# Optimization experiments

Measured on AMD Instinct MI355X. Metric: run time of the kernel, lower is better.

The kernel has to match this reference:

```python
import jax, jax.numpy as jnp
import numpy as np

B, T, S = 64, 48, 48
E, H, L, V = 512, 1024, 2, 32000


def setup_inputs() -> dict:
    key = jax.random.key(0)
    ks = jax.random.split(key, 16)
    s = 0.02
    return {
        "tgt_input": jax.random.randint(ks[0], (B, T), 0, V),
        "h0": jax.random.normal(ks[1], (L, B, H), jnp.float32),
        "c0": jax.random.normal(ks[2], (L, B, H), jnp.float32),
        "encoder_output": jax.random.normal(ks[3], (B, S, H), jnp.float32),
        "src_key_padding_mask": jnp.zeros((B, S), bool),
        "embedding": jax.random.normal(ks[4], (V, E), jnp.float32) * s,
        "W_l": jax.random.normal(ks[5], (H, H), jnp.float32) * s,
        "b_l": jnp.zeros((H,), jnp.float32),
        "W_ih0": jax.random.normal(ks[6], (4 * H, E + H), jnp.float32) * s,
        "W_hh0": jax.random.normal(ks[7], (4 * H, H), jnp.float32) * s,
        "b_ih0": jnp.zeros((4 * H,), jnp.float32),
        "b_hh0": jnp.zeros((4 * H,), jnp.float32),
        "W_ih1": jax.random.normal(ks[8], (4 * H, H), jnp.float32) * s,
        "W_hh1": jax.random.normal(ks[9], (4 * H, H), jnp.float32) * s,
        "b_ih1": jnp.zeros((4 * H,), jnp.float32),
        "b_hh1": jnp.zeros((4 * H,), jnp.float32),
    }


def _lstm_cell(x, h, c, W_ih, W_hh, b_ih, b_hh):
    # PyTorch gate order: i, f, g, o
    gates = x @ W_ih.T + b_ih + h @ W_hh.T + b_hh  # [B, 4H]
    i, f, g, o = jnp.split(gates, 4, axis=-1)
    c_new = jax.nn.sigmoid(f) * c + jax.nn.sigmoid(i) * jnp.tanh(g)
    h_new = jax.nn.sigmoid(o) * jnp.tanh(c_new)
    return h_new, c_new


def reference(tgt_input, h0, c0, encoder_output, src_key_padding_mask,
              embedding, W_l, b_l,
              W_ih0, W_hh0, b_ih0, b_hh0,
              W_ih1, W_hh1, b_ih1, b_hh1):
    emb = embedding[tgt_input]              # [B, T, E]
    emb_t = jnp.transpose(emb, (1, 0, 2))   # [T, B, E]
    layers = ((W_ih0, W_hh0, b_ih0, b_hh0), (W_ih1, W_hh1, b_ih1, b_hh1))

    def step(carry, x_t):
        h, c = carry                        # [L, B, H] each
        # Luong attention with query = last-layer hidden state
        q = h[-1] @ W_l.T + b_l             # [B, H]
        scores = jnp.einsum('bh,bsh->bs', q, encoder_output)
        scores = jnp.where(src_key_padding_mask, -jnp.inf, scores)
        attn = jax.nn.softmax(scores, axis=-1)
        ctx = jnp.einsum('bs,bsh->bh', attn, encoder_output)  # [B, H]
        x = jnp.concatenate([x_t, ctx], axis=-1)              # [B, E+H]
        new_h, new_c = [], []
        for l, (W_ih, W_hh, b_ih, b_hh) in enumerate(layers):
            hn, cn = _lstm_cell(x, h[l], c[l], W_ih, W_hh, b_ih, b_hh)
            new_h.append(hn)
            new_c.append(cn)
            x = hn
        return (jnp.stack(new_h), jnp.stack(new_c)), x  # x = top-layer output

    (hn, cn), outs = jax.lax.scan(step, (h0, c0), emb_t)
    outputs = jnp.transpose(outs, (1, 0, 2))  # [B, T, H]
    return outputs, hn, cn
```

## Files before the change

kernel.cpp:

```cpp
#include <hip/hip_runtime.h>
#include <stdint.h>


using short8 = __attribute__((ext_vector_type(8))) short;
using f32x4  = __attribute__((ext_vector_type(4))) float;
typedef unsigned short u16;
typedef unsigned long long u64;

#define B_  64
#define T_  48
#define S_  48
#define H_  1024
#define E_  512

__device__ __forceinline__ float bf2f(u16 u) {
    union { unsigned int i; float f; } v; v.i = ((unsigned int)u) << 16; return v.f;
}
__device__ __forceinline__ u16 f2bf(float f) {
    union { float f; unsigned int i; } v; v.f = f;
    unsigned int r = v.i + 0x7fff + ((v.i >> 16) & 1);
    return (u16)(r >> 16);
}
__device__ __forceinline__ float sigm(float x) { return 1.f / (1.f + __expf(-x)); }


__global__ void cast_copy(u16* __restrict__ dst, int dld, int doff,
                          const float* __restrict__ src, int sld, int soff,
                          int rows, int colshift) {
    int cols = 1 << colshift;
    int total = rows << colshift;
    for (int i = blockIdx.x * blockDim.x + threadIdx.x; i < total;
         i += gridDim.x * blockDim.x) {
        int r = i >> colshift, c = i & (cols - 1);
        dst[(size_t)r * dld + doff + c] = f2bf(src[(size_t)r * sld + soff + c]);
    }
}

__global__ void transpose_cast(u16* __restrict__ dst, const float* __restrict__ src) {
    int idx = blockIdx.x * blockDim.x + threadIdx.x;
    int r = idx >> 10, c = idx & 1023;
    dst[idx] = f2bf(src[(size_t)c * 1024 + r]);
}

__global__ void embed_gather(u16* __restrict__ embA, const float* __restrict__ emb,
                             const int* __restrict__ tgt) {
    int row = blockIdx.x;
    int t = row >> 6, b = row & 63;
    int id = tgt[b * T_ + t];
    const float* s = emb + (size_t)id * E_;
    u16* d = embA + (size_t)row * E_;
    for (int e = threadIdx.x; e < E_; e += blockDim.x) d[e] = f2bf(s[e]);
}

__global__ void sbias_kernel(float* __restrict__ sbias, const float* __restrict__ enc,
                             const float* __restrict__ b_l) {
    int r = blockIdx.x, lane = threadIdx.x;
    const float* e = enc + (size_t)r * H_;
    float acc = 0.f;
    for (int k = lane; k < H_; k += 64) acc += b_l[k] * e[k];
    for (int o = 32; o; o >>= 1) acc += __shfl_xor(acc, o);
    if (lane == 0) sbias[r] = acc;
}

__global__ void init_state(u16* __restrict__ xa0_0, u16* __restrict__ xa1_0,
                           const float* __restrict__ h0) {
    int i = blockIdx.x * blockDim.x + threadIdx.x;
    int l = i >> 16, rem = i & 65535, b = rem >> 10, c = rem & 1023;
    u16 hb = f2bf(h0[i]);
    if (l == 0) xa0_0[b * 2048 + 1024 + c] = hb;
    else        xa1_0[b * 2048 + 1024 + c] = hb;
}

__global__ __launch_bounds__(256) void gemm64(
    const u16* __restrict__ A, const u16* __restrict__ W, u16* __restrict__ D,
    const float* __restrict__ bias1, const float* __restrict__ bias2,
    int N, int Kd)
{
    __shared__ float part[4][64][65];
    int tid = threadIdx.x, w = tid >> 6, lane = tid & 63;
    int hf = lane >> 4, q = lane & 15;
    int n0 = blockIdx.x * 64, m0 = blockIdx.y * 64;
    int ks = Kd >> 2;
    int kb = w * ks + hf * 8;
    const u16* ap = A + (size_t)(m0 + q) * Kd + kb;
    const u16* wp = W + (size_t)(n0 + q) * Kd + kb;
    f32x4 acc[4][4] = {};
    for (int k0 = 0; k0 < ks; k0 += 32) {
        short8 bf[4], af[4];
#pragma unroll
        for (int n = 0; n < 4; ++n) bf[n] = *(const short8*)(wp + (size_t)n * 16 * Kd + k0);
#pragma unroll
        for (int m = 0; m < 4; ++m) af[m] = *(const short8*)(ap + (size_t)m * 16 * Kd + k0);
#pragma unroll
        for (int m = 0; m < 4; ++m)
#pragma unroll
            for (int n = 0; n < 4; ++n)
                acc[m][n] = __builtin_amdgcn_mfma_f32_16x16x32_bf16(af[m], bf[n], acc[m][n], 0, 0, 0);
    }
#pragma unroll
    for (int m = 0; m < 4; ++m)
#pragma unroll
        for (int n = 0; n < 4; ++n)
#pragma unroll
            for (int r = 0; r < 4; ++r)
                part[w][m * 16 + hf * 4 + r][n * 16 + q] = acc[m][n][r];
    __syncthreads();
#pragma unroll
    for (int k = 0; k < 16; ++k) {
        int o = tid + k * 256;
        int row = o >> 6, col = o & 63;
        float v = part[0][row][col] + part[1][row][col]
                + part[2][row][col] + part[3][row][col];
        if (bias1) v += bias1[n0 + col] + bias2[n0 + col];
        D[(size_t)(m0 + row) * N + n0 + col] = f2bf(v);
    }
}


struct PParams {
    const float *W_ih0, *W_hh0, *W_ih1, *W_hh1;
    const u16  *preG, *encW, *encB;
    const float *sbias, *b_ih1, *b_hh1, *c0in;
    const unsigned char* mask;
    u16 *XA0, *XA1;
    float *out, *hn0, *hn1, *cn0, *cn1;
    unsigned *cnt, *flags;
};

__device__ __forceinline__ void gridbar(unsigned* cnt, unsigned* flags, int ep) {
    __syncthreads();
    const int tid = threadIdx.x;
    const int g = (blockIdx.x & 7) * 8 + ((blockIdx.x >> 3) & 7);
    if (tid == 0)
        __hip_atomic_fetch_add(&cnt[g * 256 + ep], 1u,
                               __ATOMIC_RELAXED, __HIP_MEMORY_SCOPE_AGENT);
    if (blockIdx.x == 0) {
        if (tid < 64) {
            int spin = 0;
            for (;;) {
                unsigned v = __hip_atomic_load(&cnt[tid * 256 + ep],
                                               __ATOMIC_RELAXED,
                                               __HIP_MEMORY_SCOPE_AGENT);
                if (__ballot(v >= 4u) == ~0ull) break;
                __builtin_amdgcn_s_sleep(1);
                if (++spin > (1 << 20)) break;
            }
            __hip_atomic_store(&flags[tid * 256 + ep], 1u,
                               __ATOMIC_RELAXED, __HIP_MEMORY_SCOPE_AGENT);
        }
    } else if (tid == 0) {
        int spin = 0;
        while (!__hip_atomic_load(&flags[g * 256 + ep], __ATOMIC_RELAXED,
                                  __HIP_MEMORY_SCOPE_AGENT)) {
            __builtin_amdgcn_s_sleep(1);
            if (++spin > (1 << 20)) break;
        }
    }
    asm volatile("" ::: "memory");
    __syncthreads();
}

__global__ void __launch_bounds__(256, 1) decoder_persistent(PParams P) {
    __shared__ u16 wlds[2][4096][8];
    __shared__ union {
        struct { float h1f[1056]; float sc[48][4]; float pr[48]; } at;
        float gates[64][20];
    } sm;

    const int tid = threadIdx.x, blk = blockIdx.x;
    const int w = tid >> 6, lane = tid & 63, g4 = lane >> 4, q = lane & 15;
    const int b2 = tid >> 2, j2 = tid & 3;
    const int colg = blk * 4 + j2;

    {
        int r = tid & 15, cb = tid >> 4;
        int grow = (r >> 2) * 1024 + blk * 4 + (r & 3);
#pragma unroll
        for (int l = 0; l < 2; ++l) {
            const float* Sa = l ? P.W_ih1 : P.W_ih0;
            const float* Sb = l ? P.W_hh1 : P.W_hh0;
            int sld  = l ? 1024 : 1536;
            int soff = l ? 0 : 512;
            for (int it = 0; it < 16; ++it) {
                int c = cb + it * 16;
                int k = c * 8;
                const float* src = (k < 1024)
                    ? (Sa + (size_t)grow * sld + soff + k)
                    : (Sb + (size_t)grow * 1024 + (k - 1024));
                float4 x0 = *(const float4*)(src);
                float4 x1 = *(const float4*)(src + 4);
                short8 v;
                v[0] = f2bf(x0.x); v[1] = f2bf(x0.y); v[2] = f2bf(x0.z); v[3] = f2bf(x0.w);
                v[4] = f2bf(x1.x); v[5] = f2bf(x1.y); v[6] = f2bf(x1.z); v[7] = f2bf(x1.w);
                *(short8*)&wlds[l][c * 16 + r][0] = v;
            }
        }
    }
    float bsum[4];
#pragma unroll
    for (int g = 0; g < 4; ++g)
        bsum[g] = P.b_ih1[g * 1024 + colg] + P.b_hh1[g * 1024 + colg];
    float c0r = P.c0in[b2 * 1024 + colg];
    float c1r = P.c0in[65536 + b2 * 1024 + colg];

    const int ab = (blk & 7) * 8 + ((blk >> 3) & 7);
    const int aq = blk >> 6;
    int ep = 0;
    int t = 0;

    auto gemm_half = [&](const u16* Abase, int layer, int kbase, f32x4 seed) -> f32x4 {
        const u16* ap = Abase + (size_t)(w * 16 + q) * 2048 + kbase + g4 * 8;
        short8 xa[32];
#pragma unroll
        for (int kk = 0; kk < 32; ++kk)
            xa[kk] = *(const short8*)(ap + kk * 32);
        f32x4 a0 = seed, a1 = {}, a2 = {}, a3 = {};
        const int cbs = (kbase >> 3) + g4;
#pragma unroll
        for (int kk = 0; kk < 32; kk += 4) {
            a0 = __builtin_amdgcn_mfma_f32_16x16x32_bf16(
                xa[kk + 0], *(const short8*)&wlds[layer][(cbs + (kk + 0) * 4) * 16 + q][0], a0, 0, 0, 0);
            a1 = __builtin_amdgcn_mfma_f32_16x16x32_bf16(
                xa[kk + 1], *(const short8*)&wlds[layer][(cbs + (kk + 1) * 4) * 16 + q][0], a1, 0, 0, 0);
            a2 = __builtin_amdgcn_mfma_f32_16x16x32_bf16(
                xa[kk + 2], *(const short8*)&wlds[layer][(cbs + (kk + 2) * 4) * 16 + q][0], a2, 0, 0, 0);
            a3 = __builtin_amdgcn_mfma_f32_16x16x32_bf16(
                xa[kk + 3], *(const short8*)&wlds[layer][(cbs + (kk + 3) * 4) * 16 + q][0], a3, 0, 0, 0);
        }
        return (a0 + a1) + (a2 + a3);
    };

    auto lstm_phase = [&](const u16* Abase, int layer, f32x4 seed,
                          float add0, float add1, float add2, float add3,
                          float& creg, u16* dA, u16* dB, float* outp,
                          float* hnO, float* cnO, int doLast) {
        f32x4 g = gemm_half(Abase, layer, 0, seed);
#pragma unroll
        for (int r = 0; r < 4; ++r) sm.gates[w * 16 + g4 * 4 + r][q] = g[r];
        __syncthreads();
        float gi = sm.gates[b2][j2]      + add0;
        float gf = sm.gates[b2][4 + j2]  + add1;
        float gg = sm.gates[b2][8 + j2]  + add2;
        float go = sm.gates[b2][12 + j2] + add3;
        float cnew = sigm(gf) * creg + sigm(gi) * tanhf(gg);
        float hnew = sigm(go) * tanhf(cnew);
        creg = cnew;
        ((u16*)&sm.gates[b2][16])[j2] = f2bf(hnew);
        if (outp) outp[(size_t)(b2 * T_ + t) * H_ + colg] = hnew;
        if (doLast) { hnO[b2 * 1024 + colg] = hnew; cnO[b2 * 1024 + colg] = cnew; }
        __syncthreads();
        if (tid < 64) {
            u64 pk;
            __builtin_memcpy(&pk, (const u16*)&sm.gates[tid][16], 8);
            __hip_atomic_store((u64*)(dA + tid * 2048 + blk * 4), pk,
                               __ATOMIC_RELAXED, __HIP_MEMORY_SCOPE_AGENT);
            if (dB)
                __hip_atomic_store((u64*)(dB + tid * 2048 + blk * 4), pk,
                                   __ATOMIC_RELAXED, __HIP_MEMORY_SCOPE_AGENT);
        }
    };

    for (t = 0; t < T_; ++t) {
        const int last = (t == T_ - 1);
        u16* xa0c = P.XA0 + (size_t)t * 131072;
        u16* xa0n = P.XA0 + (size_t)(t + 1) * 131072;
        u16* xa1c = P.XA1 + (size_t)t * 131072;
        u16* xa1n = P.XA1 + (size_t)(t + 1) * 131072;

        for (int i = tid; i < H_; i += 256)
            sm.at.h1f[(i >> 8) * 264 + (i & 255)] = bf2f(xa1c[ab * 2048 + 1024 + i]);
        __syncthreads();
        if (tid < 192) {
            int s = tid >> 2, kq = tid & 3;
            const u16* ew = P.encW + ((size_t)ab * S_ + s) * H_ + kq * 256;
            const float2* hp = (const float2*)(sm.at.h1f + kq * 264);
            float p0 = 0.f, p1 = 0.f, p2 = 0.f, p3 = 0.f;
#pragma unroll
            for (int k = 0; k < 256; k += 32) {
                short8 v0 = *(const short8*)(ew + k);
                short8 v1 = *(const short8*)(ew + k + 8);
                short8 v2 = *(const short8*)(ew + k + 16);
                short8 v3 = *(const short8*)(ew + k + 24);
#pragma unroll
                for (int e = 0; e < 8; e += 2) {
                    float2 h0v = hp[(k >> 1) + (e >> 1)];
                    p0 += h0v.x * bf2f(((u16*)&v0)[e]) + h0v.y * bf2f(((u16*)&v0)[e + 1]);
                    float2 h1v = hp[(k >> 1) + 4 + (e >> 1)];
                    p1 += h1v.x * bf2f(((u16*)&v1)[e]) + h1v.y * bf2f(((u16*)&v1)[e + 1]);
                    float2 h2v = hp[(k >> 1) + 8 + (e >> 1)];
                    p2 += h2v.x * bf2f(((u16*)&v2)[e]) + h2v.y * bf2f(((u16*)&v2)[e + 1]);
                    float2 h3v = hp[(k >> 1) + 12 + (e >> 1)];
                    p3 += h3v.x * bf2f(((u16*)&v3)[e]) + h3v.y * bf2f(((u16*)&v3)[e + 1]);
                }
            }
            sm.at.sc[s][kq] = (p0 + p1) + (p2 + p3);
        }
        __syncthreads();
        if (tid < 64) {
            float v = -3.0e38f;
            if (tid < S_) {
                v = sm.at.sc[tid][0] + sm.at.sc[tid][1] + sm.at.sc[tid][2]
                  + sm.at.sc[tid][3] + P.sbias[ab * S_ + tid];
                if (P.mask[ab * S_ + tid]) v = -3.0e38f;
            }
            float mx = v;
            for (int o = 32; o; o >>= 1) mx = fmaxf(mx, __shfl_xor(mx, o));
            float e = (tid < S_) ? __expf(v - mx) : 0.f;
            float su = e;
            for (int o = 32; o; o >>= 1) su += __shfl_xor(su, o);
            if (tid < S_) sm.at.pr[tid] = e / su;
        }
        f32x4 g0p = gemm_half(xa0c, 0, 1024, f32x4{});
        f32x4 g1p = gemm_half(xa1c, 1, 1024, f32x4{});
        __syncthreads();
        {
            int col = aq * 256 + tid;
            const u16* eb = P.encB + (size_t)ab * S_ * H_ + col;
            float a0 = 0.f, a1 = 0.f, a2 = 0.f, a3 = 0.f;
#pragma unroll
            for (int s = 0; s < 48; s += 4) {
                a0 += sm.at.pr[s + 0] * bf2f(eb[(size_t)(s + 0) * H_]);
                a1 += sm.at.pr[s + 1] * bf2f(eb[(size_t)(s + 1) * H_]);
                a2 += sm.at.pr[s + 2] * bf2f(eb[(size_t)(s + 2) * H_]);
                a3 += sm.at.pr[s + 3] * bf2f(eb[(size_t)(s + 3) * H_]);
            }
            u16 myb = f2bf((a0 + a1) + (a2 + a3));
            int other = __shfl_xor((int)myb, 1);
            if ((tid & 1) == 0) {
                unsigned pk = (unsigned)myb | ((unsigned)(u16)other << 16);
                __hip_atomic_store((unsigned*)(xa0c + ab * 2048 + col), pk,
                                   __ATOMIC_RELAXED, __HIP_MEMORY_SCOPE_AGENT);
            }
        }
        const u16* pgp = P.preG + ((size_t)t * 64 + b2) * 4096 + colg;
        u16 pg0 = pgp[0], pg1 = pgp[1024], pg2 = pgp[2048], pg3 = pgp[3072];
        gridbar(P.cnt, P.flags, ++ep);

        lstm_phase(xa0c, 0, g0p, bf2f(pg0), bf2f(pg1), bf2f(pg2), bf2f(pg3),
                   c0r, xa1c, xa0n + 1024, nullptr, P.hn0, P.cn0, last);
        gridbar(P.cnt, P.flags, ++ep);

        lstm_phase(xa1c, 1, g1p, bsum[0], bsum[1], bsum[2], bsum[3],
                   c1r, xa1n + 1024, nullptr, P.out, P.hn1, P.cn1, last);
        gridbar(P.cnt, P.flags, ++ep);
    }
}


extern "C" void kernel_launch(void* const* d_in, const int* in_sizes, int n_in,
                              void* d_out, int out_size, void* d_ws, size_t ws_size,
                              hipStream_t stream) {
    const int*   tgt      = (const int*)d_in[0];
    const float* h0       = (const float*)d_in[1];
    const float* c0in     = (const float*)d_in[2];
    const float* enc      = (const float*)d_in[3];
    const unsigned char* mask = (const unsigned char*)d_in[4];
    const float* embedding= (const float*)d_in[5];
    const float* W_l      = (const float*)d_in[6];
    const float* b_l      = (const float*)d_in[7];
    const float* W_ih0    = (const float*)d_in[8];
    const float* W_hh0    = (const float*)d_in[9];
    const float* b_ih0    = (const float*)d_in[10];
    const float* b_hh0    = (const float*)d_in[11];
    const float* W_ih1    = (const float*)d_in[12];
    const float* W_hh1    = (const float*)d_in[13];
    const float* b_ih1    = (const float*)d_in[14];
    const float* b_hh1    = (const float*)d_in[15];
    float* out = (float*)d_out;

    char* ws = (char*)d_ws;
    u16* W0emb = (u16*)ws;               ws += (size_t)4096 * 512 * 2;
    u16* WlT   = (u16*)ws;               ws += (size_t)1024 * 1024 * 2;
    u16* embA  = (u16*)ws;               ws += (size_t)3072 * 512 * 2;
    u16* encB  = (u16*)ws;               ws += (size_t)3072 * 1024 * 2;
    u16* encWb = (u16*)ws;               ws += (size_t)3072 * 1024 * 2;
    float* sbias = (float*)ws;           ws += (size_t)3072 * 4;
    u16* preG  = (u16*)ws;               ws += (size_t)3072 * 4096 * 2;
    u16* XA0   = (u16*)ws;               ws += (size_t)49 * 131072 * 2;
    u16* XA1   = (u16*)ws;               ws += (size_t)49 * 131072 * 2;
    unsigned* bar = (unsigned*)ws;       ws += 262144;

    cast_copy<<<2048, 256, 0, stream>>>(W0emb, 512, 0, W_ih0, 1536, 0, 4096, 9);
    cast_copy<<<2048, 256, 0, stream>>>(encB, 1024, 0, enc, 1024, 0, 3072, 10);
    transpose_cast<<<4096, 256, 0, stream>>>(WlT, W_l);
    embed_gather<<<3072, 256, 0, stream>>>(embA, embedding, tgt);
    init_state<<<512, 256, 0, stream>>>(XA0, XA1, h0);
    sbias_kernel<<<3072, 64, 0, stream>>>(sbias, enc, b_l);
    gemm64<<<dim3(64, 48), 256, 0, stream>>>(embA, W0emb, preG, b_ih0, b_hh0, 4096, 512);
    gemm64<<<dim3(16, 48), 256, 0, stream>>>(encB, WlT, encWb, nullptr, nullptr, 1024, 1024);
    hipMemsetAsync(bar, 0, 262144, stream);

    PParams prm;
    prm.W_ih0 = W_ih0; prm.W_hh0 = W_hh0; prm.W_ih1 = W_ih1; prm.W_hh1 = W_hh1;
    prm.preG = preG; prm.encW = encWb; prm.encB = encB;
    prm.sbias = sbias; prm.b_ih1 = b_ih1; prm.b_hh1 = b_hh1; prm.c0in = c0in;
    prm.mask = mask;
    prm.XA0 = XA0; prm.XA1 = XA1;
    prm.out = out;
    prm.hn0 = out + 3145728; prm.hn1 = out + 3145728 + 65536;
    prm.cn0 = out + 3276800; prm.cn1 = out + 3276800 + 65536;
    prm.cnt = bar; prm.flags = bar + 16384;
    decoder_persistent<<<256, 256, 0, stream>>>(prm);

    (void)in_sizes; (void)n_in; (void)out_size; (void)ws_size;
}
```

Baseline: 1.359 ms.

## Split grid barrier into arrive/poll and overlap recurrent GEMM with barrier wait

```diff
diff --git a/kernel.cpp b/kernel.cpp
--- a/kernel.cpp
+++ b/kernel.cpp
@@ -124,35 +124,25 @@
     const unsigned char* mask;
     u16 *XA0, *XA1;
     float *out, *hn0, *hn1, *cn0, *cn1;
-    unsigned *cnt, *flags;
+    unsigned *cnt;
 };
 
-__device__ __forceinline__ void gridbar(unsigned* cnt, unsigned* flags, int ep) {
+__device__ __forceinline__ void gridarrive(unsigned* cnt, int ep, int g) {
     __syncthreads();
-    const int tid = threadIdx.x;
-    const int g = (blockIdx.x & 7) * 8 + ((blockIdx.x >> 3) & 7);
-    if (tid == 0)
+    if (threadIdx.x == 0)
         __hip_atomic_fetch_add(&cnt[g * 256 + ep], 1u,
                                __ATOMIC_RELAXED, __HIP_MEMORY_SCOPE_AGENT);
-    if (blockIdx.x == 0) {
-        if (tid < 64) {
-            int spin = 0;
-            for (;;) {
-                unsigned v = __hip_atomic_load(&cnt[tid * 256 + ep],
-                                               __ATOMIC_RELAXED,
-                                               __HIP_MEMORY_SCOPE_AGENT);
-                if (__ballot(v >= 4u) == ~0ull) break;
-                __builtin_amdgcn_s_sleep(1);
-                if (++spin > (1 << 20)) break;
-            }
-            __hip_atomic_store(&flags[tid * 256 + ep], 1u,
-                               __ATOMIC_RELAXED, __HIP_MEMORY_SCOPE_AGENT);
-        }
-    } else if (tid == 0) {
+    asm volatile("" ::: "memory");
+}
+__device__ __forceinline__ void gridpoll(unsigned* cnt, int ep) {
+    if (threadIdx.x < 64) {
         int spin = 0;
-        while (!__hip_atomic_load(&flags[g * 256 + ep], __ATOMIC_RELAXED,
-                                  __HIP_MEMORY_SCOPE_AGENT)) {
-            __builtin_amdgcn_s_sleep(1);
+        for (;;) {
+            unsigned v = __hip_atomic_load(&cnt[threadIdx.x * 256 + ep],
+                                           __ATOMIC_RELAXED,
+                                           __HIP_MEMORY_SCOPE_AGENT);
+            if (__ballot(v >= 4u) == ~0ull) break;
+            __builtin_amdgcn_s_sleep(2);
             if (++spin > (1 << 20)) break;
         }
     }
@@ -196,6 +186,7 @@
             }
         }
     }
+    __syncthreads();
     float bsum[4];
 #pragma unroll
     for (int g = 0; g < 4; ++g)
@@ -310,8 +301,6 @@
             for (int o = 32; o; o >>= 1) su += __shfl_xor(su, o);
             if (tid < S_) sm.at.pr[tid] = e / su;
         }
-        f32x4 g0p = gemm_half(xa0c, 0, 1024, f32x4{});
-        f32x4 g1p = gemm_half(xa1c, 1, 1024, f32x4{});
         __syncthreads();
         {
             int col = aq * 256 + tid;
@@ -334,15 +323,20 @@
         }
         const u16* pgp = P.preG + ((size_t)t * 64 + b2) * 4096 + colg;
         u16 pg0 = pgp[0], pg1 = pgp[1024], pg2 = pgp[2048], pg3 = pgp[3072];
-        gridbar(P.cnt, P.flags, ++ep);
+        gridarrive(P.cnt, ++ep, ab);
+        f32x4 g0p = gemm_half(xa0c, 0, 1024, f32x4{});
+        f32x4 g1p = gemm_half(xa1c, 1, 1024, f32x4{});
+        gridpoll(P.cnt, ep);
 
         lstm_phase(xa0c, 0, g0p, bf2f(pg0), bf2f(pg1), bf2f(pg2), bf2f(pg3),
                    c0r, xa1c, xa0n + 1024, nullptr, P.hn0, P.cn0, last);
-        gridbar(P.cnt, P.flags, ++ep);
+        gridarrive(P.cnt, ++ep, ab);
+        gridpoll(P.cnt, ep);
 
         lstm_phase(xa1c, 1, g1p, bsum[0], bsum[1], bsum[2], bsum[3],
                    c1r, xa1n + 1024, nullptr, P.out, P.hn1, P.cn1, last);
-        gridbar(P.cnt, P.flags, ++ep);
+        gridarrive(P.cnt, ++ep, ab);
+        gridpoll(P.cnt, ep);
     }
 }
 
@@ -399,7 +393,7 @@
     prm.out = out;
     prm.hn0 = out + 3145728; prm.hn1 = out + 3145728 + 65536;
     prm.cn0 = out + 3276800; prm.cn1 = out + 3276800 + 65536;
-    prm.cnt = bar; prm.flags = bar + 16384;
+    prm.cnt = bar;
     decoder_persistent<<<256, 256, 0, stream>>>(prm);
 
     (void)in_sizes; (void)n_in; (void)out_size; (void)ws_size;
```

Measured after the change: 1.405 ms. 1.03x slower.
